# Kernel tuning notes

Hardware: AMD Instinct MI355X
Metric: run time of the kernel (lower is better)

The kernel has to match this reference:

```python
import jax, jax.numpy as jnp
import numpy as np

N = 50000
E = 800000
D_IN = 128
D_H = 128
D_OUT = 40
BN_EPS = 1e-5


def setup_inputs() -> dict:
    key = jax.random.key(0)
    ks = jax.random.split(key, 16)
    s = lambda d: 1.0 / np.sqrt(d)
    inp = {
        "x": jax.random.normal(ks[0], (N, D_IN), jnp.float32),
        "edge_index": jax.random.randint(ks[1], (2, E), 0, N, jnp.int64),
        # conv1 MLP: Linear(D_IN,D_H) -> BN -> ReLU -> Linear(D_H,D_H) -> ReLU
        "W1a": jax.random.uniform(ks[2], (D_IN, D_H), jnp.float32, -s(D_IN), s(D_IN)),
        "b1a": jnp.zeros((D_H,), jnp.float32),
        "g1": jnp.ones((D_H,), jnp.float32),
        "be1": jnp.zeros((D_H,), jnp.float32),
        "W2a": jax.random.uniform(ks[3], (D_H, D_H), jnp.float32, -s(D_H), s(D_H)),
        "b2a": jnp.zeros((D_H,), jnp.float32),
        # conv2 MLP
        "W1b": jax.random.uniform(ks[4], (D_H, D_H), jnp.float32, -s(D_H), s(D_H)),
        "b1b": jnp.zeros((D_H,), jnp.float32),
        "g2": jnp.ones((D_H,), jnp.float32),
        "be2": jnp.zeros((D_H,), jnp.float32),
        "W2b": jax.random.uniform(ks[5], (D_H, D_H), jnp.float32, -s(D_H), s(D_H)),
        "b2b": jnp.zeros((D_H,), jnp.float32),
        # head
        "Wl1": jax.random.uniform(ks[6], (D_H, D_H), jnp.float32, -s(D_H), s(D_H)),
        "bl1": jnp.zeros((D_H,), jnp.float32),
        "Wl2": jax.random.uniform(ks[7], (D_H, D_OUT), jnp.float32, -s(D_H), s(D_H)),
        "bl2": jnp.zeros((D_OUT,), jnp.float32),
    }
    return inp


def _batchnorm(h, gamma, beta):
    # BatchNorm1d in training mode: biased batch stats over the node dim
    mu = h.mean(axis=0)
    var = h.var(axis=0)
    return (h - mu) * jax.lax.rsqrt(var + BN_EPS) * gamma + beta


def _gin_conv(x, src, dst, W1, b1, gamma, beta, W2, b2):
    # sum-aggregation over neighbors (eps = 0): (1+eps)*x + sum_{j in N(i)} x_j
    agg = x + jax.ops.segment_sum(x[src], dst, num_segments=N)
    h = agg @ W1 + b1
    h = jax.nn.relu(_batchnorm(h, gamma, beta))
    return jax.nn.relu(h @ W2 + b2)


def reference(x, edge_index, W1a, b1a, g1, be1, W2a, b2a,
              W1b, b1b, g2, be2, W2b, b2b, Wl1, bl1, Wl2, bl2):
    src, dst = edge_index[0], edge_index[1]
    h = jax.nn.relu(_gin_conv(x, src, dst, W1a, b1a, g1, be1, W2a, b2a))
    # dropout is a no-op here (deterministic reference / eval)
    h = _gin_conv(h, src, dst, W1b, b1b, g2, be2, W2b, b2b)
    h = jax.nn.relu(h @ Wl1 + bl1)
    h = h @ Wl2 + bl2
    return jax.nn.log_softmax(h, axis=1)
```

## Files before the change

kernel.cpp:

```cpp
#include <hip/hip_runtime.h>
#include <math.h>

#define NN 50000
#define NE 800000
#define DD 128
#define DOUT 40
#define BN_EPS_F 1e-5f
#define BSTRIDE 64
#define NPX (NN / 8)
#define EPB 1024
#define BUCKET_BLOCKS (((NE + EPB - 1) / EPB) * 8)
#define X2BF_BLOCKS 6250
#define WPREP_BLOCKS ((5 * 16384 + 255) / 256)

typedef __attribute__((ext_vector_type(8))) short bf16x8;
typedef __attribute__((ext_vector_type(4))) float f32x4;

static __device__ __forceinline__ unsigned short f2bf(float f) {
  unsigned u = __float_as_uint(f);
  unsigned r = (u + 0x7FFFu + ((u >> 16) & 1u)) >> 16;
  return (unsigned short)r;
}
static __device__ __forceinline__ float bf2f(unsigned short u) {
  return __uint_as_float((unsigned)u << 16);
}

__global__ void k_zero(int* __restrict__ cnt, float* __restrict__ stats) {
  int i = blockIdx.x * 256 + threadIdx.x;
  if (i < NN) cnt[i] = 0;
  if (i < 4 * DD) stats[i] = 0.f;
}

__global__ void k_bucketprep(const int* __restrict__ srcI, const int* __restrict__ dstI,
                             int* __restrict__ cnt, unsigned short* __restrict__ bkt,
                             const float4* __restrict__ x, ushort4* __restrict__ xb,
                             const float* __restrict__ W0, const float* __restrict__ W1,
                             const float* __restrict__ W2, const float* __restrict__ W3,
                             const float* __restrict__ W4, unsigned short* __restrict__ wf) {
  int b = blockIdx.x;
  if (b < BUCKET_BLOCKS) {
    int xcd = b & 7;
    int chunk = b >> 3;
    int lo = xcd * NPX, hi = lo + NPX;
    int e0 = chunk * EPB + threadIdx.x * 4;
    if (e0 < NE) {
      int4 d4 = *(const int4*)(dstI + e0);
      int4 s4 = *(const int4*)(srcI + e0);
      int dd[4] = {d4.x, d4.y, d4.z, d4.w};
      int ss[4] = {s4.x, s4.y, s4.z, s4.w};
#pragma unroll
      for (int i = 0; i < 4; i++) {
        int d = dd[i];
        if (d >= lo && d < hi) {
          int r = atomicAdd(&cnt[d], 1);
          if (r < BSTRIDE) bkt[(size_t)d * BSTRIDE + r] = (unsigned short)ss[i];
        }
      }
    }
  } else if (b < BUCKET_BLOCKS + X2BF_BLOCKS) {
    int i = (b - BUCKET_BLOCKS) * 256 + threadIdx.x;
    if (i < NN * 32) {
      float4 v = x[i];
      ushort4 r;
      r.x = f2bf(v.x); r.y = f2bf(v.y); r.z = f2bf(v.z); r.w = f2bf(v.w);
      xb[i] = r;
    }
  } else {
    int fid = (b - BUCKET_BLOCKS - X2BF_BLOCKS) * 256 + threadIdx.x;
    if (fid >= 5 * 16384) return;
    int g = fid >> 14;
    int r = fid & 16383;
    int i = r & 7;
    int lane = (r >> 3) & 63;
    int ks = (r >> 9) & 3;
    int ct = r >> 11;
    int k = ks * 32 + (lane >> 4) * 8 + i;
    int col = ct * 16 + (lane & 15);
    const float* Wp = (g == 0) ? W0 : (g == 1) ? W1 : (g == 2) ? W2 : (g == 3) ? W3 : W4;
    float w = Wp[k * DD + col];
    unsigned short hi = f2bf(w);
    unsigned short lo = f2bf(w - bf2f(hi));
    wf[g * 32768 + r] = hi;
    wf[g * 32768 + 16384 + r] = lo;
  }
}

__global__ void k_aggr_bf(const ushort4* __restrict__ x, const int* __restrict__ cnt,
                          const unsigned short* __restrict__ bkt,
                          ushort4* __restrict__ out) {
  int tid = blockIdx.x * 256 + threadIdx.x;
  int node = tid >> 5;
  if (node >= NN) return;
  int c = tid & 31;
  int cn = cnt[node];
  cn = (cn < BSTRIDE) ? cn : BSTRIDE;
  const unsigned short* bp = bkt + (size_t)node * BSTRIDE;
  ushort4 sv = x[node * 32 + c];
  float ax = bf2f(sv.x), ay = bf2f(sv.y), az = bf2f(sv.z), aw = bf2f(sv.w);
  int j = 0;
  for (; j + 3 < cn; j += 4) {
    int s0 = bp[j], s1 = bp[j + 1], s2 = bp[j + 2], s3 = bp[j + 3];
    ushort4 v0 = x[s0 * 32 + c];
    ushort4 v1 = x[s1 * 32 + c];
    ushort4 v2 = x[s2 * 32 + c];
    ushort4 v3 = x[s3 * 32 + c];
    ax += bf2f(v0.x) + bf2f(v1.x) + bf2f(v2.x) + bf2f(v3.x);
    ay += bf2f(v0.y) + bf2f(v1.y) + bf2f(v2.y) + bf2f(v3.y);
    az += bf2f(v0.z) + bf2f(v1.z) + bf2f(v2.z) + bf2f(v3.z);
    aw += bf2f(v0.w) + bf2f(v1.w) + bf2f(v2.w) + bf2f(v3.w);
  }
  for (; j < cn; j++) {
    int s0 = bp[j];
    ushort4 v0 = x[s0 * 32 + c];
    ax += bf2f(v0.x); ay += bf2f(v0.y); az += bf2f(v0.z); aw += bf2f(v0.w);
  }
  ushort4 r;
  r.x = f2bf(ax); r.y = f2bf(ay); r.z = f2bf(az); r.w = f2bf(aw);
  out[node * 32 + c] = r;
}

template<bool BN_IN, bool RELU_OUT, bool STATS_OUT, bool HEAD>
__global__ __launch_bounds__(512) void k_mgemm(
    const unsigned short* __restrict__ in, const unsigned short* __restrict__ wf,
    const float* __restrict__ bias, float* __restrict__ outF,
    unsigned short* __restrict__ outB,
    const float* __restrict__ statsIn, float* __restrict__ statsOut,
    const float* __restrict__ gamma, const float* __restrict__ beta,
    const float* __restrict__ W2h, const float* __restrict__ b2h) {
  __shared__ __align__(16) char smem[65536];
  __shared__ float scs[DD], shs[DD], lbias[DD], ls[DD], lq[DD];
  short* lw = (short*)smem;
  int tid = threadIdx.x;
  int lane = tid & 63, wv = tid >> 6;
  int rbase = blockIdx.x * 128 + wv * 16;
  int kq = (lane >> 4) * 8;

  bf16x8 araw[4];
  {
    int row = rbase + (lane & 15);
    bool v = row < NN;
    const unsigned short* ap = in + (size_t)row * DD + kq;
    bf16x8 zz = {0, 0, 0, 0, 0, 0, 0, 0};
#pragma unroll
    for (int ks = 0; ks < 4; ks++)
      araw[ks] = v ? *(const bf16x8*)(ap + ks * 32) : zz;
  }

  {
    const float4* src = (const float4*)wf;
    float4* dst = (float4*)lw;
#pragma unroll
    for (int it = 0; it < 8; it++) dst[it * 512 + tid] = src[it * 512 + tid];
  }
  if (tid < DD) {
    lbias[tid] = bias[tid];
    if (STATS_OUT) { ls[tid] = 0.f; lq[tid] = 0.f; }
    if (BN_IN) {
      float mu  = statsIn[tid] * (1.0f / NN);
      float var = statsIn[DD + tid] * (1.0f / NN) - mu * mu;
      float sc  = gamma[tid] * rsqrtf(var + BN_EPS_F);
      scs[tid] = sc;
      shs[tid] = beta[tid] - mu * sc;
    }
  }
  __syncthreads();

  bf16x8 ahi[4];
  if constexpr (BN_IN) {
#pragma unroll
    for (int ks = 0; ks < 4; ks++) {
      const float4* s4 = (const float4*)&scs[ks * 32 + kq];
      const float4* h4 = (const float4*)&shs[ks * 32 + kq];
      float4 sa = s4[0], sb = s4[1], ha = h4[0], hb = h4[1];
      float ss[8] = {sa.x, sa.y, sa.z, sa.w, sb.x, sb.y, sb.z, sb.w};
      float hh[8] = {ha.x, ha.y, ha.z, ha.w, hb.x, hb.y, hb.z, hb.w};
      bf16x8 h;
#pragma unroll
      for (int i = 0; i < 8; i++) {
        float xv = fmaxf(bf2f((unsigned short)araw[ks][i]) * ss[i] + hh[i], 0.f);
        h[i] = (short)f2bf(xv);
      }
      ahi[ks] = h;
    }
  } else {
#pragma unroll
    for (int ks = 0; ks < 4; ks++) ahi[ks] = araw[ks];
  }

  f32x4 acc[8];
#pragma unroll
  for (int ct = 0; ct < 8; ct++) acc[ct] = (f32x4){0.f, 0.f, 0.f, 0.f};
  const bf16x8* lwv = (const bf16x8*)lw;
#pragma unroll
  for (int ks = 0; ks < 4; ks++) {
#pragma unroll
    for (int ct = 0; ct < 8; ct++) {
      bf16x8 bh = lwv[(ct * 4 + ks) * 64 + lane];
      bf16x8 bl = lwv[2048 + (ct * 4 + ks) * 64 + lane];
      acc[ct] = __builtin_amdgcn_mfma_f32_16x16x32_bf16(ahi[ks], bh, acc[ct], 0, 0, 0);
      acc[ct] = __builtin_amdgcn_mfma_f32_16x16x32_bf16(ahi[ks], bl, acc[ct], 0, 0, 0);
    }
  }

  if constexpr (!HEAD) {
    int r0 = rbase + (lane >> 4) * 4;
#pragma unroll
    for (int ct = 0; ct < 8; ct++) {
      int col = ct * 16 + (lane & 15);
      float bb = lbias[col];
      float s = 0.f, q = 0.f;
#pragma unroll
      for (int j = 0; j < 4; j++) {
        int row = r0 + j;
        if (row < NN) {
          float v = acc[ct][j] + bb;
          if (RELU_OUT) v = fmaxf(v, 0.f);
          outB[(size_t)row * DD + col] = f2bf(v);
          if (STATS_OUT) { s += v; q += v * v; }
        }
      }
      if (STATS_OUT) {
        s += __shfl_xor(s, 16); s += __shfl_xor(s, 32);
        q += __shfl_xor(q, 16); q += __shfl_xor(q, 32);
        if ((lane >> 4) == 0) {
          atomicAdd(&ls[col], s);
          atomicAdd(&lq[col], q);
        }
      }
    }
    if (STATS_OUT) {
      __syncthreads();
      if (tid < DD) {
        atomicAdd(&statsOut[tid], ls[tid]);
        atomicAdd(&statsOut[DD + tid], lq[tid]);
      }
    }
  } else {
    unsigned short* hs = (unsigned short*)smem;
    float* W2s = (float*)(smem + 33792);
    __syncthreads();
    {
      int lr0 = wv * 16 + (lane >> 4) * 4;
#pragma unroll
      for (int ct = 0; ct < 8; ct++) {
        int col = ct * 16 + (lane & 15);
        float bb = lbias[col];
#pragma unroll
        for (int j = 0; j < 4; j++) {
          float v = fmaxf(acc[ct][j] + bb, 0.f);
          hs[(lr0 + j) * 132 + col] = f2bf(v);
        }
      }
      const float4* W2g = (const float4*)W2h;
      float4* W2s4 = (float4*)W2s;
#pragma unroll
      for (int it = 0; it < 3; it++) {
        int idx = it * 512 + tid;
        if (idx < 1280) W2s4[idx] = W2g[idx];
      }
    }
    __syncthreads();
    int lrow = tid >> 2, q = tid & 3;
    int grow = blockIdx.x * 128 + lrow;
    float a2[40];
#pragma unroll
    for (int j = 0; j < 40; j++) a2[j] = 0.f;
    for (int kk = 0; kk < 32; kk++) {
      int k = kk * 4 + q;
      float hv = bf2f(hs[lrow * 132 + k]);
      const float4* wrow = (const float4*)(W2s + k * DOUT);
#pragma unroll
      for (int j4 = 0; j4 < 10; j4++) {
        float4 w = wrow[j4];
        a2[j4 * 4 + 0] += hv * w.x;
        a2[j4 * 4 + 1] += hv * w.y;
        a2[j4 * 4 + 2] += hv * w.z;
        a2[j4 * 4 + 3] += hv * w.w;
      }
    }
#pragma unroll
    for (int j = 0; j < 40; j++) {
      a2[j] += __shfl_xor(a2[j], 1);
      a2[j] += __shfl_xor(a2[j], 2);
    }
    if (q == 0 && grow < NN) {
      const float4* b24 = (const float4*)b2h;
      float m = -INFINITY;
#pragma unroll
      for (int j4 = 0; j4 < 10; j4++) {
        float4 bb = b24[j4];
        a2[j4 * 4 + 0] += bb.x; a2[j4 * 4 + 1] += bb.y;
        a2[j4 * 4 + 2] += bb.z; a2[j4 * 4 + 3] += bb.w;
      }
#pragma unroll
      for (int j = 0; j < 40; j++) m = fmaxf(m, a2[j]);
      float s = 0.f;
#pragma unroll
      for (int j = 0; j < 40; j++) s += expf(a2[j] - m);
      float d = m + logf(s);
      float4* out4 = (float4*)(outF + (size_t)grow * DOUT);
#pragma unroll
      for (int j4 = 0; j4 < 10; j4++) {
        float4 v = make_float4(a2[j4 * 4 + 0] - d, a2[j4 * 4 + 1] - d,
                               a2[j4 * 4 + 2] - d, a2[j4 * 4 + 3] - d);
        out4[j4] = v;
      }
    }
  }
}

extern "C" void kernel_launch(void* const* d_in, const int* in_sizes, int n_in,
                              void* d_out, int out_size, void* d_ws, size_t ws_size,
                              hipStream_t stream) {
  const float* x   = (const float*)d_in[0];
  const int*   ei  = (const int*)d_in[1];
  const float* W1a = (const float*)d_in[2];
  const float* b1a = (const float*)d_in[3];
  const float* g1  = (const float*)d_in[4];
  const float* be1 = (const float*)d_in[5];
  const float* W2a = (const float*)d_in[6];
  const float* b2a = (const float*)d_in[7];
  const float* W1b = (const float*)d_in[8];
  const float* b1b = (const float*)d_in[9];
  const float* g2  = (const float*)d_in[10];
  const float* be2 = (const float*)d_in[11];
  const float* W2b = (const float*)d_in[12];
  const float* b2b = (const float*)d_in[13];
  const float* Wl1 = (const float*)d_in[14];
  const float* bl1 = (const float*)d_in[15];
  const float* Wl2 = (const float*)d_in[16];
  const float* bl2 = (const float*)d_in[17];
  float* out = (float*)d_out;

  unsigned short* bufX = (unsigned short*)d_ws;
  unsigned short* bufA = bufX + (size_t)NN * DD;
  unsigned short* bufB = bufA + (size_t)NN * DD;
  float* stats1 = (float*)(bufB + (size_t)NN * DD);
  float* stats2 = stats1 + 2 * DD;
  int*   cnt    = (int*)(stats2 + 2 * DD);
  unsigned short* bkt = (unsigned short*)(cnt + NN);
  size_t wfOff = (((size_t)(bkt + (size_t)NN * BSTRIDE) - (size_t)d_ws) + 15) & ~(size_t)15;
  unsigned short* wfrag = (unsigned short*)((char*)d_ws + wfOff);

  const int* srcI = ei;
  const int* dstI = ei + NE;

  dim3 blk(256);
  int aggrGrid = (NN * 32 + 255) / 256;
  int gemmGrid = (NN + 127) / 128;
  int bpGrid   = BUCKET_BLOCKS + X2BF_BLOCKS + WPREP_BLOCKS;
  int zeroGrid = (NN + 255) / 256;

  k_zero<<<zeroGrid, blk, 0, stream>>>(cnt, stats1);
  k_bucketprep<<<bpGrid, blk, 0, stream>>>(srcI, dstI, cnt, bkt, (const float4*)x,
                                           (ushort4*)bufX, W1a, W2a, W1b, W2b, Wl1, wfrag);

  k_aggr_bf<<<aggrGrid, blk, 0, stream>>>((const ushort4*)bufX, cnt, bkt, (ushort4*)bufA);
  k_mgemm<false, false, true, false><<<gemmGrid, 512, 0, stream>>>(
      bufA, wfrag + 0 * 32768, b1a, nullptr, bufB,
      nullptr, stats1, nullptr, nullptr, nullptr, nullptr);
  k_mgemm<true, true, false, false><<<gemmGrid, 512, 0, stream>>>(
      bufB, wfrag + 1 * 32768, b2a, nullptr, bufA,
      stats1, nullptr, g1, be1, nullptr, nullptr);
  k_aggr_bf<<<aggrGrid, blk, 0, stream>>>((const ushort4*)bufA, cnt, bkt, (ushort4*)bufB);
  k_mgemm<false, false, true, false><<<gemmGrid, 512, 0, stream>>>(
      bufB, wfrag + 2 * 32768, b1b, nullptr, bufA,
      nullptr, stats2, nullptr, nullptr, nullptr, nullptr);
  k_mgemm<true, true, false, false><<<gemmGrid, 512, 0, stream>>>(
      bufA, wfrag + 3 * 32768, b2b, nullptr, bufB,
      stats2, nullptr, g2, be2, nullptr, nullptr);
  k_mgemm<false, false, true, true><<<gemmGrid, 512, 0, stream>>>(
      bufB, wfrag + 4 * 32768, bl1, out, nullptr,
      nullptr, nullptr, nullptr, nullptr, Wl2, bl2);
}
```

Measured before the change: 203.9 us.

## Fuse each GIN conv MLP into one cooperative kernel with grid-wide BN sync

Each GIN conv's two GEMMs plus BatchNorm now run in a single cooperative kernel of 256 blocks, each handling two 128-row tiles. The first-GEMM result stays in registers while global BN statistics are gathered across a grid sync, then normalized, written to LDS and fed to the second GEMM. This removes the bf16 round trip of the intermediate activation through global memory and one launch per layer. In exchange it uses 128KB of LDS per block, needs all blocks co-resident for the grid sync, and leaves roughly one block per CU.

```diff
diff --git a/kernel.cpp b/kernel.cpp
--- a/kernel.cpp
+++ b/kernel.cpp
@@ -1,5 +1,8 @@
 #include <hip/hip_runtime.h>
+#include <hip/hip_cooperative_groups.h>
 #include <math.h>
+
+namespace cg = cooperative_groups;
 
 #define NN 50000
 #define NE 800000
@@ -12,6 +15,7 @@
 #define BUCKET_BLOCKS (((NE + EPB - 1) / EPB) * 8)
 #define X2BF_BLOCKS 6250
 #define WPREP_BLOCKS ((5 * 16384 + 255) / 256)
+#define HSTRIDE 136
 
 typedef __attribute__((ext_vector_type(8))) short bf16x8;
 typedef __attribute__((ext_vector_type(4))) float f32x4;
@@ -119,16 +123,181 @@
   out[node * 32 + c] = r;
 }
 
-template<bool BN_IN, bool RELU_OUT, bool STATS_OUT, bool HEAD>
-__global__ __launch_bounds__(512) void k_mgemm(
+__global__ __launch_bounds__(512) void k_conv(
+    const unsigned short* __restrict__ in,
+    const unsigned short* __restrict__ wf1, const float* __restrict__ b1v,
+    const unsigned short* __restrict__ wf2, const float* __restrict__ b2v,
+    const float* __restrict__ gamma, const float* __restrict__ beta,
+    float* __restrict__ stats, unsigned short* __restrict__ outB) {
+  __shared__ __align__(16) char R1[65536];
+  __shared__ __align__(16) char R2[65536];
+  __shared__ float scs[DD], shs[DD], lb1[DD], lb2[DD], ls[DD], lq[DD];
+  int tid = threadIdx.x;
+  int lane = tid & 63, wv = tid >> 6;
+  int kq = (lane >> 4) * 8;
+  int rb0 = blockIdx.x * 128 + wv * 16;
+  int rb[2] = {rb0, rb0 + 32768};
+
+  bf16x8 araw[2][4];
+  bf16x8 zz = {0, 0, 0, 0, 0, 0, 0, 0};
+#pragma unroll
+  for (int p = 0; p < 2; p++) {
+    int row = rb[p] + (lane & 15);
+    bool v = row < NN;
+    const unsigned short* ap = in + (size_t)row * DD + kq;
+#pragma unroll
+    for (int ks = 0; ks < 4; ks++)
+      araw[p][ks] = v ? *(const bf16x8*)(ap + ks * 32) : zz;
+  }
+
+  {
+    const float4* s1 = (const float4*)wf1;
+    const float4* s2 = (const float4*)wf2;
+    float4* d1 = (float4*)R1;
+    float4* d2 = (float4*)R2;
+#pragma unroll
+    for (int it = 0; it < 8; it++) {
+      d1[it * 512 + tid] = s1[it * 512 + tid];
+      d2[it * 512 + tid] = s2[it * 512 + tid];
+    }
+  }
+  if (tid < DD) {
+    lb1[tid] = b1v[tid];
+    lb2[tid] = b2v[tid];
+    ls[tid] = 0.f; lq[tid] = 0.f;
+  }
+  __syncthreads();
+
+  f32x4 acc[2][8];
+#pragma unroll
+  for (int p = 0; p < 2; p++)
+#pragma unroll
+    for (int ct = 0; ct < 8; ct++) acc[p][ct] = (f32x4){0.f, 0.f, 0.f, 0.f};
+  {
+    const bf16x8* l1 = (const bf16x8*)R1;
+#pragma unroll
+    for (int ks = 0; ks < 4; ks++) {
+#pragma unroll
+      for (int ct = 0; ct < 8; ct++) {
+        bf16x8 bh = l1[(ct * 4 + ks) * 64 + lane];
+        bf16x8 bl = l1[2048 + (ct * 4 + ks) * 64 + lane];
+        acc[0][ct] = __builtin_amdgcn_mfma_f32_16x16x32_bf16(araw[0][ks], bh, acc[0][ct], 0, 0, 0);
+        acc[0][ct] = __builtin_amdgcn_mfma_f32_16x16x32_bf16(araw[0][ks], bl, acc[0][ct], 0, 0, 0);
+        acc[1][ct] = __builtin_amdgcn_mfma_f32_16x16x32_bf16(araw[1][ks], bh, acc[1][ct], 0, 0, 0);
+        acc[1][ct] = __builtin_amdgcn_mfma_f32_16x16x32_bf16(araw[1][ks], bl, acc[1][ct], 0, 0, 0);
+      }
+    }
+  }
+
+  {
+    int fr0 = (lane >> 4) * 4;
+#pragma unroll
+    for (int ct = 0; ct < 8; ct++) {
+      int col = ct * 16 + (lane & 15);
+      float bb = lb1[col];
+      float s = 0.f, q = 0.f;
+#pragma unroll
+      for (int p = 0; p < 2; p++) {
+        int r0 = rb[p] + fr0;
+#pragma unroll
+        for (int j = 0; j < 4; j++) {
+          if (r0 + j < NN) {
+            float v = acc[p][ct][j] + bb;
+            s += v; q += v * v;
+          }
+        }
+      }
+      s += __shfl_xor(s, 16); s += __shfl_xor(s, 32);
+      q += __shfl_xor(q, 16); q += __shfl_xor(q, 32);
+      if ((lane >> 4) == 0) {
+        atomicAdd(&ls[col], s);
+        atomicAdd(&lq[col], q);
+      }
+    }
+  }
+  __syncthreads();
+  if (tid < DD) {
+    atomicAdd(&stats[tid], ls[tid]);
+    atomicAdd(&stats[DD + tid], lq[tid]);
+  }
+
+  cg::this_grid().sync();
+
+  if (tid < DD) {
+    float mu  = stats[tid] * (1.0f / NN);
+    float var = stats[DD + tid] * (1.0f / NN) - mu * mu;
+    float sc  = gamma[tid] * rsqrtf(var + BN_EPS_F);
+    scs[tid] = sc;
+    shs[tid] = beta[tid] - mu * sc;
+  }
+  __syncthreads();
+
+  unsigned short* hs = (unsigned short*)R1;
+  const bf16x8* l2 = (const bf16x8*)R2;
+#pragma unroll
+  for (int p = 0; p < 2; p++) {
+    {
+      int fr0 = (lane >> 4) * 4;
+      int lr0 = wv * 16 + fr0;
+#pragma unroll
+      for (int ct = 0; ct < 8; ct++) {
+        int col = ct * 16 + (lane & 15);
+        float sc = scs[col], sh = shs[col], bb = lb1[col];
+#pragma unroll
+        for (int j = 0; j < 4; j++) {
+          float v = fmaxf((acc[p][ct][j] + bb) * sc + sh, 0.f);
+          hs[(lr0 + j) * HSTRIDE + col] = f2bf(v);
+        }
+      }
+    }
+    __syncthreads();
+    bf16x8 a2[4];
+    {
+      int lr = wv * 16 + (lane & 15);
+#pragma unroll
+      for (int ks = 0; ks < 4; ks++)
+        a2[ks] = *(const bf16x8*)(hs + lr * HSTRIDE + ks * 32 + kq);
+    }
+    f32x4 o[8];
+#pragma unroll
+    for (int ct = 0; ct < 8; ct++) o[ct] = (f32x4){0.f, 0.f, 0.f, 0.f};
+#pragma unroll
+    for (int ks = 0; ks < 4; ks++) {
+#pragma unroll
+      for (int ct = 0; ct < 8; ct++) {
+        bf16x8 bh = l2[(ct * 4 + ks) * 64 + lane];
+        bf16x8 bl = l2[2048 + (ct * 4 + ks) * 64 + lane];
+        o[ct] = __builtin_amdgcn_mfma_f32_16x16x32_bf16(a2[ks], bh, o[ct], 0, 0, 0);
+        o[ct] = __builtin_amdgcn_mfma_f32_16x16x32_bf16(a2[ks], bl, o[ct], 0, 0, 0);
+      }
+    }
+    {
+      int fr0 = (lane >> 4) * 4;
+      int r0 = rb[p] + fr0;
+#pragma unroll
+      for (int ct = 0; ct < 8; ct++) {
+        int col = ct * 16 + (lane & 15);
+        float bb = lb2[col];
+#pragma unroll
+        for (int j = 0; j < 4; j++) {
+          int row = r0 + j;
+          if (row < NN) {
+            float v = fmaxf(o[ct][j] + bb, 0.f);
+            outB[(size_t)row * DD + col] = f2bf(v);
+          }
+        }
+      }
+    }
+    __syncthreads();
+  }
+}
+
+__global__ __launch_bounds__(512) void k_headm(
     const unsigned short* __restrict__ in, const unsigned short* __restrict__ wf,
     const float* __restrict__ bias, float* __restrict__ outF,
-    unsigned short* __restrict__ outB,
-    const float* __restrict__ statsIn, float* __restrict__ statsOut,
-    const float* __restrict__ gamma, const float* __restrict__ beta,
     const float* __restrict__ W2h, const float* __restrict__ b2h) {
   __shared__ __align__(16) char smem[65536];
-  __shared__ float scs[DD], shs[DD], lbias[DD], ls[DD], lq[DD];
+  __shared__ float lbias[DD];
   short* lw = (short*)smem;
   int tid = threadIdx.x;
   int lane = tid & 63, wv = tid >> 6;
@@ -145,47 +314,14 @@
     for (int ks = 0; ks < 4; ks++)
       araw[ks] = v ? *(const bf16x8*)(ap + ks * 32) : zz;
   }
-
   {
     const float4* src = (const float4*)wf;
     float4* dst = (float4*)lw;
 #pragma unroll
     for (int it = 0; it < 8; it++) dst[it * 512 + tid] = src[it * 512 + tid];
   }
-  if (tid < DD) {
-    lbias[tid] = bias[tid];
-    if (STATS_OUT) { ls[tid] = 0.f; lq[tid] = 0.f; }
-    if (BN_IN) {
-      float mu  = statsIn[tid] * (1.0f / NN);
-      float var = statsIn[DD + tid] * (1.0f / NN) - mu * mu;
-      float sc  = gamma[tid] * rsqrtf(var + BN_EPS_F);
-      scs[tid] = sc;
-      shs[tid] = beta[tid] - mu * sc;
-    }
-  }
-  __syncthreads();
-
-  bf16x8 ahi[4];
-  if constexpr (BN_IN) {
-#pragma unroll
-    for (int ks = 0; ks < 4; ks++) {
-      const float4* s4 = (const float4*)&scs[ks * 32 + kq];
-      const float4* h4 = (const float4*)&shs[ks * 32 + kq];
-      float4 sa = s4[0], sb = s4[1], ha = h4[0], hb = h4[1];
-      float ss[8] = {sa.x, sa.y, sa.z, sa.w, sb.x, sb.y, sb.z, sb.w};
-      float hh[8] = {ha.x, ha.y, ha.z, ha.w, hb.x, hb.y, hb.z, hb.w};
-      bf16x8 h;
-#pragma unroll
-      for (int i = 0; i < 8; i++) {
-        float xv = fmaxf(bf2f((unsigned short)araw[ks][i]) * ss[i] + hh[i], 0.f);
-        h[i] = (short)f2bf(xv);
-      }
-      ahi[ks] = h;
-    }
-  } else {
-#pragma unroll
-    for (int ks = 0; ks < 4; ks++) ahi[ks] = araw[ks];
-  }
+  if (tid < DD) lbias[tid] = bias[tid];
+  __syncthreads();
 
   f32x4 acc[8];
 #pragma unroll
@@ -197,114 +333,79 @@
     for (int ct = 0; ct < 8; ct++) {
       bf16x8 bh = lwv[(ct * 4 + ks) * 64 + lane];
       bf16x8 bl = lwv[2048 + (ct * 4 + ks) * 64 + lane];
-      acc[ct] = __builtin_amdgcn_mfma_f32_16x16x32_bf16(ahi[ks], bh, acc[ct], 0, 0, 0);
-      acc[ct] = __builtin_amdgcn_mfma_f32_16x16x32_bf16(ahi[ks], bl, acc[ct], 0, 0, 0);
-    }
-  }
-
-  if constexpr (!HEAD) {
-    int r0 = rbase + (lane >> 4) * 4;
+      acc[ct] = __builtin_amdgcn_mfma_f32_16x16x32_bf16(araw[ks], bh, acc[ct], 0, 0, 0);
+      acc[ct] = __builtin_amdgcn_mfma_f32_16x16x32_bf16(araw[ks], bl, acc[ct], 0, 0, 0);
+    }
+  }
+
+  unsigned short* hs = (unsigned short*)smem;
+  float* W2s = (float*)(smem + 33792);
+  __syncthreads();
+  {
+    int lr0 = wv * 16 + (lane >> 4) * 4;
 #pragma unroll
     for (int ct = 0; ct < 8; ct++) {
       int col = ct * 16 + (lane & 15);
       float bb = lbias[col];
-      float s = 0.f, q = 0.f;
 #pragma unroll
       for (int j = 0; j < 4; j++) {
-        int row = r0 + j;
-        if (row < NN) {
-          float v = acc[ct][j] + bb;
-          if (RELU_OUT) v = fmaxf(v, 0.f);
-          outB[(size_t)row * DD + col] = f2bf(v);
-          if (STATS_OUT) { s += v; q += v * v; }
-        }
-      }
-      if (STATS_OUT) {
-        s += __shfl_xor(s, 16); s += __shfl_xor(s, 32);
-        q += __shfl_xor(q, 16); q += __shfl_xor(q, 32);
-        if ((lane >> 4) == 0) {
-          atomicAdd(&ls[col], s);
-          atomicAdd(&lq[col], q);
-        }
-      }
-    }
-    if (STATS_OUT) {
-      __syncthreads();
-      if (tid < DD) {
-        atomicAdd(&statsOut[tid], ls[tid]);
-        atomicAdd(&statsOut[DD + tid], lq[tid]);
-      }
-    }
-  } else {
-    unsigned short* hs = (unsigned short*)smem;
-    float* W2s = (float*)(smem + 33792);
-    __syncthreads();
-    {
-      int lr0 = wv * 16 + (lane >> 4) * 4;
-#pragma unroll
-      for (int ct = 0; ct < 8; ct++) {
-        int col = ct * 16 + (lane & 15);
-        float bb = lbias[col];
-#pragma unroll
-        for (int j = 0; j < 4; j++) {
-          float v = fmaxf(acc[ct][j] + bb, 0.f);
-          hs[(lr0 + j) * 132 + col] = f2bf(v);
-        }
-      }
-      const float4* W2g = (const float4*)W2h;
-      float4* W2s4 = (float4*)W2s;
-#pragma unroll
-      for (int it = 0; it < 3; it++) {
-        int idx = it * 512 + tid;
-        if (idx < 1280) W2s4[idx] = W2g[idx];
-      }
-    }
-    __syncthreads();
-    int lrow = tid >> 2, q = tid & 3;
-    int grow = blockIdx.x * 128 + lrow;
-    float a2[40];
-#pragma unroll
-    for (int j = 0; j < 40; j++) a2[j] = 0.f;
-    for (int kk = 0; kk < 32; kk++) {
-      int k = kk * 4 + q;
-      float hv = bf2f(hs[lrow * 132 + k]);
-      const float4* wrow = (const float4*)(W2s + k * DOUT);
-#pragma unroll
-      for (int j4 = 0; j4 < 10; j4++) {
-        float4 w = wrow[j4];
-        a2[j4 * 4 + 0] += hv * w.x;
-        a2[j4 * 4 + 1] += hv * w.y;
-        a2[j4 * 4 + 2] += hv * w.z;
-        a2[j4 * 4 + 3] += hv * w.w;
-      }
-    }
-#pragma unroll
-    for (int j = 0; j < 40; j++) {
-      a2[j] += __shfl_xor(a2[j], 1);
-      a2[j] += __shfl_xor(a2[j], 2);
-    }
-    if (q == 0 && grow < NN) {
-      const float4* b24 = (const float4*)b2h;
-      float m = -INFINITY;
-#pragma unroll
-      for (int j4 = 0; j4 < 10; j4++) {
-        float4 bb = b24[j4];
-        a2[j4 * 4 + 0] += bb.x; a2[j4 * 4 + 1] += bb.y;
-        a2[j4 * 4 + 2] += bb.z; a2[j4 * 4 + 3] += bb.w;
-      }
-#pragma unroll
-      for (int j = 0; j < 40; j++) m = fmaxf(m, a2[j]);
-      float s = 0.f;
-#pragma unroll
-      for (int j = 0; j < 40; j++) s += expf(a2[j] - m);
-      float d = m + logf(s);
-      float4* out4 = (float4*)(outF + (size_t)grow * DOUT);
-#pragma unroll
-      for (int j4 = 0; j4 < 10; j4++) {
-        float4 v = make_float4(a2[j4 * 4 + 0] - d, a2[j4 * 4 + 1] - d,
-                               a2[j4 * 4 + 2] - d, a2[j4 * 4 + 3] - d);
-        out4[j4] = v;
-      }
+        float v = fmaxf(acc[ct][j] + bb, 0.f);
+        hs[(lr0 + j) * 132 + col] = f2bf(v);
+      }
+    }
+    const float4* W2g = (const float4*)W2h;
+    float4* W2s4 = (float4*)W2s;
+#pragma unroll
+    for (int it = 0; it < 3; it++) {
+      int idx = it * 512 + tid;
+      if (idx < 1280) W2s4[idx] = W2g[idx];
+    }
+  }
+  __syncthreads();
+  int lrow = tid >> 2, q = tid & 3;
+  int grow = blockIdx.x * 128 + lrow;
+  float a2[40];
+#pragma unroll
+  for (int j = 0; j < 40; j++) a2[j] = 0.f;
+  for (int kk = 0; kk < 32; kk++) {
+    int k = kk * 4 + q;
+    float hv = bf2f(hs[lrow * 132 + k]);
+    const float4* wrow = (const float4*)(W2s + k * DOUT);
+#pragma unroll
+    for (int j4 = 0; j4 < 10; j4++) {
+      float4 w = wrow[j4];
+      a2[j4 * 4 + 0] += hv * w.x;
+      a2[j4 * 4 + 1] += hv * w.y;
+      a2[j4 * 4 + 2] += hv * w.z;
+      a2[j4 * 4 + 3] += hv * w.w;
+    }
+  }
+#pragma unroll
+  for (int j = 0; j < 40; j++) {
+    a2[j] += __shfl_xor(a2[j], 1);
+    a2[j] += __shfl_xor(a2[j], 2);
+  }
+  if (q == 0 && grow < NN) {
+    const float4* b24 = (const float4*)b2h;
+    float m = -INFINITY;
+#pragma unroll
+    for (int j4 = 0; j4 < 10; j4++) {
+      float4 bb = b24[j4];
+      a2[j4 * 4 + 0] += bb.x; a2[j4 * 4 + 1] += bb.y;
+      a2[j4 * 4 + 2] += bb.z; a2[j4 * 4 + 3] += bb.w;
+    }
+#pragma unroll
+    for (int j = 0; j < 40; j++) m = fmaxf(m, a2[j]);
+    float s = 0.f;
+#pragma unroll
+    for (int j = 0; j < 40; j++) s += expf(a2[j] - m);
+    float d = m + logf(s);
+    float4* out4 = (float4*)(outF + (size_t)grow * DOUT);
+#pragma unroll
+    for (int j4 = 0; j4 < 10; j4++) {
+      float4 v = make_float4(a2[j4 * 4 + 0] - d, a2[j4 * 4 + 1] - d,
+                             a2[j4 * 4 + 2] - d, a2[j4 * 4 + 3] - d);
+      out4[j4] = v;
     }
   }
 }
@@ -347,7 +448,7 @@
 
   dim3 blk(256);
   int aggrGrid = (NN * 32 + 255) / 256;
-  int gemmGrid = (NN + 127) / 128;
+  int headGrid = (NN + 127) / 128;
   int bpGrid   = BUCKET_BLOCKS + X2BF_BLOCKS + WPREP_BLOCKS;
   int zeroGrid = (NN + 255) / 256;
 
@@ -356,20 +457,32 @@
                                            (ushort4*)bufX, W1a, W2a, W1b, W2b, Wl1, wfrag);
 
   k_aggr_bf<<<aggrGrid, blk, 0, stream>>>((const ushort4*)bufX, cnt, bkt, (ushort4*)bufA);
-  k_mgemm<false, false, true, false><<<gemmGrid, 512, 0, stream>>>(
-      bufA, wfrag + 0 * 32768, b1a, nullptr, bufB,
-      nullptr, stats1, nullptr, nullptr, nullptr, nullptr);
-  k_mgemm<true, true, false, false><<<gemmGrid, 512, 0, stream>>>(
-      bufB, wfrag + 1 * 32768, b2a, nullptr, bufA,
-      stats1, nullptr, g1, be1, nullptr, nullptr);
-  k_aggr_bf<<<aggrGrid, blk, 0, stream>>>((const ushort4*)bufA, cnt, bkt, (ushort4*)bufB);
-  k_mgemm<false, false, true, false><<<gemmGrid, 512, 0, stream>>>(
-      bufB, wfrag + 2 * 32768, b1b, nullptr, bufA,
-      nullptr, stats2, nullptr, nullptr, nullptr, nullptr);
-  k_mgemm<true, true, false, false><<<gemmGrid, 512, 0, stream>>>(
-      bufA, wfrag + 3 * 32768, b2b, nullptr, bufB,
-      stats2, nullptr, g2, be2, nullptr, nullptr);
-  k_mgemm<false, false, true, true><<<gemmGrid, 512, 0, stream>>>(
-      bufB, wfrag + 4 * 32768, bl1, out, nullptr,
-      nullptr, nullptr, nullptr, nullptr, Wl2, bl2);
-}
+  {
+    const unsigned short* cin = bufA;
+    const unsigned short* cw1 = wfrag + 0 * 32768;
+    const float* cb1 = b1a;
+    const unsigned short* cw2 = wfrag + 1 * 32768;
+    const float* cb2 = b2a;
+    const float* cga = g1;
+    const float* cbe = be1;
+    float* cst = stats1;
+    unsigned short* cout = bufB;
+    void* cargs[] = {&cin, &cw1, &cb1, &cw2, &cb2, &cga, &cbe, &cst, &cout};
+    hipLaunchCooperativeKernel((const void*)k_conv, dim3(256), dim3(512), cargs, 0, stream);
+  }
+  k_aggr_bf<<<aggrGrid, blk, 0, stream>>>((const ushort4*)bufB, cnt, bkt, (ushort4*)bufA);
+  {
+    const unsigned short* cin = bufA;
+    const unsigned short* cw1 = wfrag + 2 * 32768;
+    const float* cb1 = b1b;
+    const unsigned short* cw2 = wfrag + 3 * 32768;
+    const float* cb2 = b2b;
+    const float* cga = g2;
+    const float* cbe = be2;
+    float* cst = stats2;
+    unsigned short* cout = bufB;
+    void* cargs[] = {&cin, &cw1, &cb1, &cw2, &cb2, &cga, &cbe, &cst, &cout};
+    hipLaunchCooperativeKernel((const void*)k_conv, dim3(256), dim3(512), cargs, 0, stream);
+  }
+  k_headm<<<headGrid, 512, 0, stream>>>(bufB, wfrag + 4 * 32768, bl1, out, Wl2, bl2);
+}
```

After: 261.0 us. +28.0%, slower.

## Shrink per-node buckets with overflow list and load GEMM weights directly into LDS

Applied to the files above, without the earlier changes.

Halves the fixed per-node neighbor bucket stride from 64 to 32 and spills edges beyond that into a global overflow list. Aggregation scans that list linearly for high-degree nodes. This cuts bucket memory footprint and improves locality for the average-degree-16 graph. It also issues the weight-fragment copy into shared memory via global_load_lds, ahead of the A-row loads, so it overlaps and skips the register round trip. The risk is the linear overflow scan if many nodes exceed 32 neighbours; with Poisson(16) degrees that should be rare.

```diff
diff --git a/kernel.cpp b/kernel.cpp
--- a/kernel.cpp
+++ b/kernel.cpp
@@ -6,7 +6,8 @@
 #define DD 128
 #define DOUT 40
 #define BN_EPS_F 1e-5f
-#define BSTRIDE 64
+#define BSTRIDE 32
+#define OVF_MAX 8192
 #define NPX (NN / 8)
 #define EPB 1024
 #define BUCKET_BLOCKS (((NE + EPB - 1) / EPB) * 8)
@@ -25,14 +26,23 @@
   return __uint_as_float((unsigned)u << 16);
 }
 
-__global__ void k_zero(int* __restrict__ cnt, float* __restrict__ stats) {
+static __device__ __forceinline__ void gload_lds16(const void* g, void* l) {
+  __builtin_amdgcn_global_load_lds(
+      (const __attribute__((address_space(1))) void*)g,
+      (__attribute__((address_space(3))) void*)l, 16, 0, 0);
+}
+
+__global__ void k_zero(int* __restrict__ cnt, float* __restrict__ stats,
+                       int* __restrict__ ovfc) {
   int i = blockIdx.x * 256 + threadIdx.x;
   if (i < NN) cnt[i] = 0;
   if (i < 4 * DD) stats[i] = 0.f;
+  if (i == 0) ovfc[0] = 0;
 }
 
 __global__ void k_bucketprep(const int* __restrict__ srcI, const int* __restrict__ dstI,
                              int* __restrict__ cnt, unsigned short* __restrict__ bkt,
+                             int* __restrict__ ovfc, unsigned* __restrict__ ovf,
                              const float4* __restrict__ x, ushort4* __restrict__ xb,
                              const float* __restrict__ W0, const float* __restrict__ W1,
                              const float* __restrict__ W2, const float* __restrict__ W3,
@@ -53,7 +63,12 @@
         int d = dd[i];
         if (d >= lo && d < hi) {
           int r = atomicAdd(&cnt[d], 1);
-          if (r < BSTRIDE) bkt[(size_t)d * BSTRIDE + r] = (unsigned short)ss[i];
+          if (r < BSTRIDE) {
+            bkt[(size_t)d * BSTRIDE + r] = (unsigned short)ss[i];
+          } else {
+            int o = atomicAdd(ovfc, 1);
+            if (o < OVF_MAX) ovf[o] = ((unsigned)d << 16) | (unsigned)ss[i];
+          }
         }
       }
     }
@@ -87,18 +102,19 @@
 
 __global__ void k_aggr_bf(const ushort4* __restrict__ x, const int* __restrict__ cnt,
                           const unsigned short* __restrict__ bkt,
+                          const int* __restrict__ ovfc, const unsigned* __restrict__ ovf,
                           ushort4* __restrict__ out) {
   int tid = blockIdx.x * 256 + threadIdx.x;
   int node = tid >> 5;
   if (node >= NN) return;
   int c = tid & 31;
   int cn = cnt[node];
-  cn = (cn < BSTRIDE) ? cn : BSTRIDE;
+  int ce = (cn < BSTRIDE) ? cn : BSTRIDE;
   const unsigned short* bp = bkt + (size_t)node * BSTRIDE;
   ushort4 sv = x[node * 32 + c];
   float ax = bf2f(sv.x), ay = bf2f(sv.y), az = bf2f(sv.z), aw = bf2f(sv.w);
   int j = 0;
-  for (; j + 3 < cn; j += 4) {
+  for (; j + 3 < ce; j += 4) {
     int s0 = bp[j], s1 = bp[j + 1], s2 = bp[j + 2], s3 = bp[j + 3];
     ushort4 v0 = x[s0 * 32 + c];
     ushort4 v1 = x[s1 * 32 + c];
@@ -109,10 +125,21 @@
     az += bf2f(v0.z) + bf2f(v1.z) + bf2f(v2.z) + bf2f(v3.z);
     aw += bf2f(v0.w) + bf2f(v1.w) + bf2f(v2.w) + bf2f(v3.w);
   }
-  for (; j < cn; j++) {
+  for (; j < ce; j++) {
     int s0 = bp[j];
     ushort4 v0 = x[s0 * 32 + c];
     ax += bf2f(v0.x); ay += bf2f(v0.y); az += bf2f(v0.z); aw += bf2f(v0.w);
+  }
+  if (cn > BSTRIDE) {
+    int no = ovfc[0];
+    if (no > OVF_MAX) no = OVF_MAX;
+    for (int o = 0; o < no; o++) {
+      unsigned pr = ovf[o];
+      if ((int)(pr >> 16) == node) {
+        ushort4 v0 = x[(int)(pr & 0xFFFFu) * 32 + c];
+        ax += bf2f(v0.x); ay += bf2f(v0.y); az += bf2f(v0.z); aw += bf2f(v0.w);
+      }
+    }
   }
   ushort4 r;
   r.x = f2bf(ax); r.y = f2bf(ay); r.z = f2bf(az); r.w = f2bf(aw);
@@ -135,6 +162,15 @@
   int rbase = blockIdx.x * 128 + wv * 16;
   int kq = (lane >> 4) * 8;
 
+  {
+    const float4* src = (const float4*)wf;
+    float4* dst = (float4*)lw;
+    int wbase = tid & ~63;
+#pragma unroll
+    for (int it = 0; it < 8; it++)
+      gload_lds16(src + it * 512 + tid, dst + it * 512 + wbase);
+  }
+
   bf16x8 araw[4];
   {
     int row = rbase + (lane & 15);
@@ -146,12 +182,6 @@
       araw[ks] = v ? *(const bf16x8*)(ap + ks * 32) : zz;
   }
 
-  {
-    const float4* src = (const float4*)wf;
-    float4* dst = (float4*)lw;
-#pragma unroll
-    for (int it = 0; it < 8; it++) dst[it * 512 + tid] = src[it * 512 + tid];
-  }
   if (tid < DD) {
     lbias[tid] = bias[tid];
     if (STATS_OUT) { ls[tid] = 0.f; lq[tid] = 0.f; }
@@ -338,7 +368,9 @@
   float* stats1 = (float*)(bufB + (size_t)NN * DD);
   float* stats2 = stats1 + 2 * DD;
   int*   cnt    = (int*)(stats2 + 2 * DD);
-  unsigned short* bkt = (unsigned short*)(cnt + NN);
+  int*   ovfc   = cnt + NN;
+  unsigned* ovf = (unsigned*)(ovfc + 4);
+  unsigned short* bkt = (unsigned short*)(ovf + OVF_MAX);
   size_t wfOff = (((size_t)(bkt + (size_t)NN * BSTRIDE) - (size_t)d_ws) + 15) & ~(size_t)15;
   unsigned short* wfrag = (unsigned short*)((char*)d_ws + wfOff);
 
@@ -351,18 +383,21 @@
   int bpGrid   = BUCKET_BLOCKS + X2BF_BLOCKS + WPREP_BLOCKS;
   int zeroGrid = (NN + 255) / 256;
 
-  k_zero<<<zeroGrid, blk, 0, stream>>>(cnt, stats1);
-  k_bucketprep<<<bpGrid, blk, 0, stream>>>(srcI, dstI, cnt, bkt, (const float4*)x,
-                                           (ushort4*)bufX, W1a, W2a, W1b, W2b, Wl1, wfrag);
-
-  k_aggr_bf<<<aggrGrid, blk, 0, stream>>>((const ushort4*)bufX, cnt, bkt, (ushort4*)bufA);
+  k_zero<<<zeroGrid, blk, 0, stream>>>(cnt, stats1, ovfc);
+  k_bucketprep<<<bpGrid, blk, 0, stream>>>(srcI, dstI, cnt, bkt, ovfc, ovf,
+                                           (const float4*)x, (ushort4*)bufX,
+                                           W1a, W2a, W1b, W2b, Wl1, wfrag);
+
+  k_aggr_bf<<<aggrGrid, blk, 0, stream>>>((const ushort4*)bufX, cnt, bkt, ovfc, ovf,
+                                          (ushort4*)bufA);
   k_mgemm<false, false, true, false><<<gemmGrid, 512, 0, stream>>>(
       bufA, wfrag + 0 * 32768, b1a, nullptr, bufB,
       nullptr, stats1, nullptr, nullptr, nullptr, nullptr);
   k_mgemm<true, true, false, false><<<gemmGrid, 512, 0, stream>>>(
       bufB, wfrag + 1 * 32768, b2a, nullptr, bufA,
       stats1, nullptr, g1, be1, nullptr, nullptr);
-  k_aggr_bf<<<aggrGrid, blk, 0, stream>>>((const ushort4*)bufA, cnt, bkt, (ushort4*)bufB);
+  k_aggr_bf<<<aggrGrid, blk, 0, stream>>>((const ushort4*)bufA, cnt, bkt, ovfc, ovf,
+                                          (ushort4*)bufB);
   k_mgemm<false, false, true, false><<<gemmGrid, 512, 0, stream>>>(
       bufB, wfrag + 2 * 32768, b1b, nullptr, bufA,
       nullptr, stats2, nullptr, nullptr, nullptr, nullptr);
```

Result: no change. 203.0 us (-0.4%).
